# Kernel optimization log

Hardware: AMD Instinct MI355X
Metric: run time of the kernel (lower is better)

## Reference

```python
import jax, jax.numpy as jnp
import numpy as np

D_MODEL, FFN, N_EXP = 1024, 4096, 8
BS, L = 4, 2048


def setup_inputs() -> dict:
    key = jax.random.key(0)
    ks = jax.random.split(key, 7)
    s = 0.02
    return {
        "x": jax.random.normal(ks[0], (BS, L, D_MODEL), dtype=jnp.float32),
        "gate_w": s * jax.random.normal(ks[1], (D_MODEL, N_EXP), dtype=jnp.float32),
        "gate_b": jnp.zeros((N_EXP,), dtype=jnp.float32),
        "W1": s * jax.random.normal(ks[2], (N_EXP, D_MODEL, FFN), dtype=jnp.float32),
        "b1": jnp.zeros((N_EXP, FFN), dtype=jnp.float32),
        "W2": s * jax.random.normal(ks[3], (N_EXP, FFN, D_MODEL), dtype=jnp.float32),
        "b2": jnp.zeros((N_EXP, D_MODEL), dtype=jnp.float32),
    }


def reference(x, gate_w, gate_b, W1, b1, W2, b2):
    # gate logits [bs, l, E]; NOTE: original applies Softmax(dim=1) -> over seq dim
    logits = jnp.einsum("bld,de->ble", x, gate_w) + gate_b
    probs = jax.nn.softmax(logits, axis=1)  # faithful to nn.Softmax(dim=1)
    idx = jnp.argmax(probs, axis=-1)  # top-1 expert per token, [bs, l]
    # topk_weights are computed in the original but never applied to output.
    out = jnp.zeros_like(x)
    for e in range(N_EXP):  # fixed small expert loop (structurally distinct weights)
        h = jax.nn.gelu(jnp.einsum("bld,df->blf", x, W1[e]) + b1[e], approximate=False)
        y = jnp.einsum("blf,fd->bld", h, W2[e]) + b2[e]
        out = out + jnp.where((idx == e)[..., None], y, jnp.float32(0.0))
    return out
```

## Files before the change

kernel.cpp:

```cpp
#include <hip/hip_runtime.h>
#include <hip/hip_bf16.h>

typedef unsigned short u16;
typedef unsigned int u32;

using bf16x8 = __attribute__((ext_vector_type(8))) short;
using f32x4  = __attribute__((ext_vector_type(4))) float;

static constexpr int TOK  = 8192;
static constexpr int SEQ  = 2048;
static constexpr int DM   = 1024;
static constexpr int FF   = 4096;
static constexpr int NE   = 8;
static constexpr int MAXT = 72;
static constexpr int KS2  = 4;
static constexpr int NWG1 = MAXT * (FF/128);
static constexpr int NWG2 = MAXT * (DM/128) * KS2;

static constexpr size_t O_LOGITS = 0;
static constexpr size_t O_M      = 262144;
static constexpr size_t O_Z      = O_M + 128;
static constexpr size_t O_CNT    = O_Z + 128;
static constexpr size_t O_CUR    = O_CNT + 64;
static constexpr size_t O_OFF    = O_CUR + 64;
static constexpr size_t O_DESC   = 263168;
static constexpr size_t O_PERM   = 266240;
static constexpr size_t O_IDX    = 299008;
static constexpr size_t O_XG     = 524288;
static constexpr size_t O_W1T    = O_XG  + (size_t)TOK*DM*2;
static constexpr size_t O_W2T    = O_W1T + (size_t)NE*DM*FF*2;
static constexpr size_t O_H      = O_W2T + (size_t)NE*DM*FF*2;

__device__ __forceinline__ u16 f2bf(float f){
  __hip_bfloat16 h = __float2bfloat16(f);
  return *reinterpret_cast<u16*>(&h);
}

__device__ __forceinline__ void gld_lds16(const void* g, void* l){
  __builtin_amdgcn_global_load_lds((const __attribute__((address_space(1))) void*)g,
                                   (__attribute__((address_space(3))) void*)l, 16, 0, 0);
}

__device__ __forceinline__ float gelu_f(float v){
  float u = v * fmaf(v*v, 0.044715f, 1.0f) * 0.7978845608f;
  float ex = __builtin_amdgcn_exp2f(u * -2.885390082f);
  return v * __builtin_amdgcn_rcpf(1.0f + ex);
}

__global__ void k_gate(const float* __restrict__ x, const float* __restrict__ gw,
                       const float* __restrict__ gb, float* __restrict__ logits){
  __shared__ float sgw[NE*DM];
  for (int i = threadIdx.x; i < DM*NE; i += 256){
    int d = i >> 3, e = i & 7;
    sgw[e*DM + d] = gw[i];
  }
  __syncthreads();
  int wave = threadIdx.x >> 6, lane = threadIdx.x & 63;
  int t = blockIdx.x * 4 + wave;
  const float4* xr = (const float4*)(x + (size_t)t * DM);
  float acc[NE];
#pragma unroll
  for (int e = 0; e < NE; ++e) acc[e] = 0.f;
#pragma unroll
  for (int k = 0; k < 4; ++k){
    int v4 = k*64 + lane;
    float4 v = xr[v4];
#pragma unroll
    for (int e = 0; e < NE; ++e){
      const float4 g = *(const float4*)&sgw[e*DM + v4*4];
      acc[e] = fmaf(v.x, g.x, fmaf(v.y, g.y, fmaf(v.z, g.z, fmaf(v.w, g.w, acc[e]))));
    }
  }
#pragma unroll
  for (int off = 32; off; off >>= 1)
#pragma unroll
    for (int e = 0; e < NE; ++e) acc[e] += __shfl_xor(acc[e], off);
  if (lane == 0){
#pragma unroll
    for (int e = 0; e < NE; ++e) logits[(size_t)t*NE + e] = acc[e] + gb[e];
  }
}

__global__ void k_lse(const float* __restrict__ logits, float* __restrict__ mOut,
                      float* __restrict__ zOut){
  int be = blockIdx.x;
  int b = be >> 3, e = be & 7;
  const float* base = logits + ((size_t)b*SEQ)*NE + e;
  float m = -INFINITY;
  for (int l = threadIdx.x; l < SEQ; l += 256) m = fmaxf(m, base[(size_t)l*NE]);
  __shared__ float red[8];
#pragma unroll
  for (int off = 32; off; off >>= 1) m = fmaxf(m, __shfl_xor(m, off));
  if ((threadIdx.x & 63) == 0) red[threadIdx.x >> 6] = m;
  __syncthreads();
  m = fmaxf(fmaxf(red[0], red[1]), fmaxf(red[2], red[3]));
  float s = 0.f;
  for (int l = threadIdx.x; l < SEQ; l += 256) s += expf(base[(size_t)l*NE] - m);
#pragma unroll
  for (int off = 32; off; off >>= 1) s += __shfl_xor(s, off);
  if ((threadIdx.x & 63) == 0) red[4 + (threadIdx.x >> 6)] = s;
  __syncthreads();
  if (threadIdx.x == 0){ mOut[be] = m; zOut[be] = red[4]+red[5]+red[6]+red[7]; }
}

__global__ void k_route(const float* __restrict__ logits, const float* __restrict__ m,
                        const float* __restrict__ z, u32* __restrict__ cnt,
                        int* __restrict__ idx){
  int t = blockIdx.x*256 + threadIdx.x;
  int b = t >> 11;
  const float* lr = logits + (size_t)t*NE;
  float best = -INFINITY; int be = 0;
#pragma unroll
  for (int e = 0; e < NE; ++e){
    float p = expf(lr[e] - m[b*NE + e]) / z[b*NE + e];
    if (p > best){ best = p; be = e; }
  }
  idx[t] = be;
  atomicAdd(&cnt[be], 1u);
}

__global__ void k_plan(const u32* __restrict__ cnt, int* __restrict__ off,
                       int4* __restrict__ desc, u32* __restrict__ cur){
  if (threadIdx.x == 0){
    int offs[NE+1]; int o = 0;
    for (int e = 0; e < NE; ++e){ offs[e] = o; o += (int)cnt[e]; }
    offs[NE] = o;
    int nt = 0;
    for (int e = 0; e < NE; ++e){
      int c = (int)cnt[e];
      for (int s = 0; s < c; s += 128)
        desc[nt++] = make_int4(e, offs[e] + s, min(128, c - s), 0);
      off[e] = offs[e]; cur[e] = 0u;
    }
    off[NE] = offs[NE];
    for (int i = nt; i < MAXT; ++i) desc[i] = make_int4(-1, 0, 0, 0);
  }
}

__global__ void k_scatter(const int* __restrict__ idx, const int* __restrict__ off,
                          u32* __restrict__ cur, int* __restrict__ perm){
  int t = blockIdx.x*256 + threadIdx.x;
  int e = idx[t];
  int pos = off[e] + (int)atomicAdd(&cur[e], 1u);
  perm[pos] = t;
}

__global__ void k_gather(const float* __restrict__ x, const int* __restrict__ perm,
                         const int* __restrict__ idx, const float* __restrict__ b2,
                         u16* __restrict__ Xg, float* __restrict__ out){
  int p = blockIdx.x;
  int t = perm[p];
  int e = idx[t];
  const float4* src = (const float4*)(x + (size_t)t*DM);
  float4 v = src[threadIdx.x];
  uint2 o;
  o.x = (u32)f2bf(v.x) | ((u32)f2bf(v.y) << 16);
  o.y = (u32)f2bf(v.z) | ((u32)f2bf(v.w) << 16);
  *(uint2*)(Xg + (size_t)p*DM + threadIdx.x*4) = o;
  float4 bv = ((const float4*)(b2 + (size_t)e*DM))[threadIdx.x];
  ((float4*)(out + (size_t)t*DM))[threadIdx.x] = bv;
}

__global__ void k_trans(const float* __restrict__ in, u16* __restrict__ out,
                        int R, int C){
  __shared__ float tile[64][65];
  int e = blockIdx.z;
  int r0 = blockIdx.x*64, c0 = blockIdx.y*64;
  const float* src = in + ((size_t)e*R + r0)*C + c0;
  int lr = threadIdx.x >> 4, lc = (threadIdx.x & 15) * 4;
#pragma unroll
  for (int i = 0; i < 4; ++i){
    float4 v = *(const float4*)(src + (size_t)(lr + i*16)*C + lc);
    tile[lr + i*16][lc+0] = v.x; tile[lr + i*16][lc+1] = v.y;
    tile[lr + i*16][lc+2] = v.z; tile[lr + i*16][lc+3] = v.w;
  }
  __syncthreads();
  u16* dst = out + ((size_t)e*C + c0)*R + r0;
  int rr = (threadIdx.x & 7) * 8;
  int ocb = threadIdx.x >> 3;
#pragma unroll
  for (int p = 0; p < 2; ++p){
    int oc = ocb + p*32;
    u16 w[8];
#pragma unroll
    for (int k = 0; k < 8; ++k) w[k] = f2bf(tile[rr + k][oc]);
    uint4 o;
    o.x = (u32)w[0] | ((u32)w[1] << 16);
    o.y = (u32)w[2] | ((u32)w[3] << 16);
    o.z = (u32)w[4] | ((u32)w[5] << 16);
    o.w = (u32)w[6] | ((u32)w[7] << 16);
    *(uint4*)(dst + (size_t)oc*R + rr) = o;
  }
}


__global__ __launch_bounds__(512) void k_ffn1(const u16* __restrict__ Xg,
    const u16* __restrict__ W1T, const float* __restrict__ b1,
    u16* __restrict__ H, const int4* __restrict__ desc){
  int pid = blockIdx.x;
  int pid_sw = (pid & 7) * (NWG1/8) + (pid >> 3);
  int ng  = pid_sw / (MAXT*8);
  int rem = pid_sw - ng*(MAXT*8);
  int mt  = rem >> 3;
  int n0  = (ng*8 + (rem & 7)) * 128;
  int4 dd = desc[mt];
  int e = dd.x; if (e < 0) return;
  int m0 = dd.y, valid = dd.z;
  __shared__ __align__(16) u16 lA[2][128*64];
  __shared__ __align__(16) u16 lB[2][128*64];
  int tid = threadIdx.x, lane = tid & 63, wave = tid >> 6;
  int wr = wave >> 1, wc = wave & 1;
  const u16* Bsrc = W1T + ((size_t)e*FF + n0)*DM;
  f32x4 acc[2][4] = {};

  auto stage = [&](int buf, int kt){
    int k0 = kt * 64;
#pragma unroll
    for (int c = 0; c < 2; ++c){
      int idx = tid + c*512;
      int r = idx >> 3, s = idx & 7;
      int sp = (s ^ (r & 7)) * 8;
      int ra = m0 + r; if (ra > TOK-1) ra = TOK-1;
      gld_lds16(Xg   + (size_t)ra*DM + k0 + sp, (char*)&lA[buf][0] + idx*16);
      gld_lds16(Bsrc + (size_t)r *DM + k0 + sp, (char*)&lB[buf][0] + idx*16);
    }
  };

  stage(0, 0);
  __syncthreads();
  const int KT = DM / 64;
  for (int kt = 0; kt < KT; ++kt){
    int cur = kt & 1;
    if (kt + 1 < KT) stage(cur ^ 1, kt + 1);
    const char* cA = (const char*)&lA[cur][0];
    const char* cB = (const char*)&lB[cur][0];
    bf16x8 a[2][2], b[4][2];
#pragma unroll
    for (int m = 0; m < 2; ++m){
      int R = wr*32 + m*16 + (lane & 15);
#pragma unroll
      for (int h = 0; h < 2; ++h){
        int slot = (h*4 + (lane >> 4)) ^ (R & 7);
        a[m][h] = *(const bf16x8*)(cA + R*128 + slot*16);
      }
    }
#pragma unroll
    for (int n = 0; n < 4; ++n){
      int R = wc*64 + n*16 + (lane & 15);
#pragma unroll
      for (int h = 0; h < 2; ++h){
        int slot = (h*4 + (lane >> 4)) ^ (R & 7);
        b[n][h] = *(const bf16x8*)(cB + R*128 + slot*16);
      }
    }
#pragma unroll
    for (int m = 0; m < 2; ++m)
#pragma unroll
      for (int n = 0; n < 4; ++n){
        acc[m][n] = __builtin_amdgcn_mfma_f32_16x16x32_bf16(a[m][0], b[n][0], acc[m][n], 0,0,0);
        acc[m][n] = __builtin_amdgcn_mfma_f32_16x16x32_bf16(a[m][1], b[n][1], acc[m][n], 0,0,0);
      }
    __syncthreads();
  }

#pragma unroll
  for (int n = 0; n < 4; ++n){
    int col = n0 + wc*64 + n*16 + (lane & 15);
    float bias = b1[(size_t)e*FF + col];
#pragma unroll
    for (int m = 0; m < 2; ++m){
      int rbase = wr*32 + m*16 + ((lane >> 4) << 2);
#pragma unroll
      for (int j = 0; j < 4; ++j){
        int rit = rbase + j;
        if (rit < valid){
          float v = acc[m][n][j] + bias;
          H[(size_t)(m0 + rit)*FF + col] = f2bf(gelu_f(v));
        }
      }
    }
  }
}

__global__ __launch_bounds__(512) void k_ffn2(const u16* __restrict__ H,
    const u16* __restrict__ W2T, float* __restrict__ out,
    const int4* __restrict__ desc, const int* __restrict__ perm){
  int pid = blockIdx.x;
  int pid_sw = (pid & 7) * (NWG2/8) + (pid >> 3);
  int ks  = pid_sw / (MAXT*8);
  int rem = pid_sw - ks*(MAXT*8);
  int mt  = rem >> 3;
  int n0  = (rem & 7) * 128;
  int4 dd = desc[mt];
  int e = dd.x; if (e < 0) return;
  int m0 = dd.y, valid = dd.z;
  __shared__ __align__(16) u16 lA[2][128*64];
  __shared__ __align__(16) u16 lB[2][128*64];
  int tid = threadIdx.x, lane = tid & 63, wave = tid >> 6;
  int wr = wave >> 1, wc = wave & 1;
  const u16* Bsrc = W2T + ((size_t)e*DM + n0)*FF;
  const int kbase = ks * (FF/KS2);
  f32x4 acc[2][4] = {};

  auto stage = [&](int buf, int kt){
    int k0 = kbase + kt * 64;
#pragma unroll
    for (int c = 0; c < 2; ++c){
      int idx = tid + c*512;
      int r = idx >> 3, s = idx & 7;
      int sp = (s ^ (r & 7)) * 8;
      int ra = m0 + r; if (ra > TOK-1) ra = TOK-1;
      gld_lds16(H    + (size_t)ra*FF + k0 + sp, (char*)&lA[buf][0] + idx*16);
      gld_lds16(Bsrc + (size_t)r *FF + k0 + sp, (char*)&lB[buf][0] + idx*16);
    }
  };

  stage(0, 0);
  __syncthreads();
  const int KT = (FF/KS2) / 64;
  for (int kt = 0; kt < KT; ++kt){
    int cur = kt & 1;
    if (kt + 1 < KT) stage(cur ^ 1, kt + 1);
    const char* cA = (const char*)&lA[cur][0];
    const char* cB = (const char*)&lB[cur][0];
    bf16x8 a[2][2], b[4][2];
#pragma unroll
    for (int m = 0; m < 2; ++m){
      int R = wr*32 + m*16 + (lane & 15);
#pragma unroll
      for (int h = 0; h < 2; ++h){
        int slot = (h*4 + (lane >> 4)) ^ (R & 7);
        a[m][h] = *(const bf16x8*)(cA + R*128 + slot*16);
      }
    }
#pragma unroll
    for (int n = 0; n < 4; ++n){
      int R = wc*64 + n*16 + (lane & 15);
#pragma unroll
      for (int h = 0; h < 2; ++h){
        int slot = (h*4 + (lane >> 4)) ^ (R & 7);
        b[n][h] = *(const bf16x8*)(cB + R*128 + slot*16);
      }
    }
#pragma unroll
    for (int m = 0; m < 2; ++m)
#pragma unroll
      for (int n = 0; n < 4; ++n){
        acc[m][n] = __builtin_amdgcn_mfma_f32_16x16x32_bf16(a[m][0], b[n][0], acc[m][n], 0,0,0);
        acc[m][n] = __builtin_amdgcn_mfma_f32_16x16x32_bf16(a[m][1], b[n][1], acc[m][n], 0,0,0);
      }
    __syncthreads();
  }

#pragma unroll
  for (int m = 0; m < 2; ++m){
#pragma unroll
    for (int j = 0; j < 4; ++j){
      int rit = wr*32 + m*16 + ((lane >> 4) << 2) + j;
      if (rit < valid){
        int tok = perm[m0 + rit];
#pragma unroll
        for (int n = 0; n < 4; ++n){
          int col = n0 + wc*64 + n*16 + (lane & 15);
          unsafeAtomicAdd(&out[(size_t)tok*DM + col], acc[m][n][j]);
        }
      }
    }
  }
}

extern "C" void kernel_launch(void* const* d_in, const int* in_sizes, int n_in,
                              void* d_out, int out_size, void* d_ws, size_t ws_size,
                              hipStream_t stream){
  const float* x   = (const float*)d_in[0];
  const float* gw  = (const float*)d_in[1];
  const float* gb  = (const float*)d_in[2];
  const float* W1  = (const float*)d_in[3];
  const float* b1  = (const float*)d_in[4];
  const float* W2  = (const float*)d_in[5];
  const float* b2  = (const float*)d_in[6];
  float* out = (float*)d_out;
  char* ws = (char*)d_ws;

  float* logits = (float*)(ws + O_LOGITS);
  float* mArr   = (float*)(ws + O_M);
  float* zArr   = (float*)(ws + O_Z);
  u32*   cnt    = (u32*)  (ws + O_CNT);
  u32*   cur    = (u32*)  (ws + O_CUR);
  int*   off    = (int*)  (ws + O_OFF);
  int4*  desc   = (int4*) (ws + O_DESC);
  int*   perm   = (int*)  (ws + O_PERM);
  int*   idx    = (int*)  (ws + O_IDX);
  u16*   Xg     = (u16*)  (ws + O_XG);
  u16*   W1T    = (u16*)  (ws + O_W1T);
  u16*   W2T    = (u16*)  (ws + O_W2T);
  u16*   Hbuf   = (u16*)  (ws + O_H);

  hipMemsetAsync(ws + O_CNT, 0, 128, stream);

  k_gate   <<<TOK/4, 256, 0, stream>>>(x, gw, gb, logits);
  k_lse    <<<32,    256, 0, stream>>>(logits, mArr, zArr);
  k_route  <<<TOK/256, 256, 0, stream>>>(logits, mArr, zArr, cnt, idx);
  k_plan   <<<1,     64,  0, stream>>>(cnt, off, desc, cur);
  k_scatter<<<TOK/256, 256, 0, stream>>>(idx, off, cur, perm);
  k_gather <<<TOK,   256, 0, stream>>>(x, perm, idx, b2, Xg, out);
  k_trans  <<<dim3(DM/64, FF/64, NE), 256, 0, stream>>>(W1, W1T, DM, FF);
  k_trans  <<<dim3(FF/64, DM/64, NE), 256, 0, stream>>>(W2, W2T, FF, DM);
  k_ffn1   <<<NWG1,  512, 0, stream>>>(Xg, W1T, b1, Hbuf, desc);
  k_ffn2   <<<NWG2,  512, 0, stream>>>(Hbuf, W2T, out, desc, perm);
}
```

Measured before the change: 490.5 us.

## Enlarge FFN GEMM tiles to 256x256 with interleaved LDS loads and MFMA scheduling

Both grouped expert GEMMs move from 128x128 to 256x256 output tiles: expert segments are split into 256-row chunks and each wave now computes a 128x64 sub-tile. The main loop is reordered so B and half of A are read from LDS before the next stage's global-to-LDS prefetch is issued. The second half of A is loaded between MFMA groups, with s_setprio around the MFMAs and explicit waitcnt/barriers. The aim is higher arithmetic intensity and fewer redundant weight reads, at the cost of 128KB LDS per block, large register use, and more wasted rows in partially filled expert tiles.

```diff
diff --git a/kernel.cpp b/kernel.cpp
--- a/kernel.cpp
+++ b/kernel.cpp
@@ -12,10 +12,10 @@
 static constexpr int DM   = 1024;
 static constexpr int FF   = 4096;
 static constexpr int NE   = 8;
-static constexpr int MAXT = 72;
+static constexpr int MAXT2= 40;
 static constexpr int KS2  = 4;
-static constexpr int NWG1 = MAXT * (FF/128);
-static constexpr int NWG2 = MAXT * (DM/128) * KS2;
+static constexpr int NWG1 = MAXT2 * (FF/256);
+static constexpr int NWG2 = MAXT2 * (DM/256) * KS2;
 
 static constexpr size_t O_LOGITS = 0;
 static constexpr size_t O_M      = 262144;
@@ -23,7 +23,7 @@
 static constexpr size_t O_CNT    = O_Z + 128;
 static constexpr size_t O_CUR    = O_CNT + 64;
 static constexpr size_t O_OFF    = O_CUR + 64;
-static constexpr size_t O_DESC   = 263168;
+static constexpr size_t O_DESC2  = 264320;
 static constexpr size_t O_PERM   = 266240;
 static constexpr size_t O_IDX    = 299008;
 static constexpr size_t O_XG     = 524288;
@@ -120,20 +120,20 @@
 }
 
 __global__ void k_plan(const u32* __restrict__ cnt, int* __restrict__ off,
-                       int4* __restrict__ desc, u32* __restrict__ cur){
+                       int4* __restrict__ desc2, u32* __restrict__ cur){
   if (threadIdx.x == 0){
     int offs[NE+1]; int o = 0;
     for (int e = 0; e < NE; ++e){ offs[e] = o; o += (int)cnt[e]; }
     offs[NE] = o;
-    int nt = 0;
+    int nt2 = 0;
     for (int e = 0; e < NE; ++e){
       int c = (int)cnt[e];
-      for (int s = 0; s < c; s += 128)
-        desc[nt++] = make_int4(e, offs[e] + s, min(128, c - s), 0);
+      for (int s = 0; s < c; s += 256)
+        desc2[nt2++] = make_int4(e, offs[e] + s, min(256, c - s), 0);
       off[e] = offs[e]; cur[e] = 0u;
     }
     off[NE] = offs[NE];
-    for (int i = nt; i < MAXT; ++i) desc[i] = make_int4(-1, 0, 0, 0);
+    for (int i = nt2; i < MAXT2; ++i) desc2[i] = make_int4(-1, 0, 0, 0);
   }
 }
 
@@ -194,29 +194,31 @@
 }
 
 
-__global__ __launch_bounds__(512) void k_ffn1(const u16* __restrict__ Xg,
+__global__ __launch_bounds__(512, 2) void k_ffn1(const u16* __restrict__ Xg,
     const u16* __restrict__ W1T, const float* __restrict__ b1,
-    u16* __restrict__ H, const int4* __restrict__ desc){
+    u16* __restrict__ H, const int4* __restrict__ desc2){
   int pid = blockIdx.x;
   int pid_sw = (pid & 7) * (NWG1/8) + (pid >> 3);
-  int ng  = pid_sw / (MAXT*8);
-  int rem = pid_sw - ng*(MAXT*8);
-  int mt  = rem >> 3;
-  int n0  = (ng*8 + (rem & 7)) * 128;
-  int4 dd = desc[mt];
+  int mt = pid_sw % MAXT2;
+  int n0 = (pid_sw / MAXT2) * 256;
+  int4 dd = desc2[mt];
   int e = dd.x; if (e < 0) return;
   int m0 = dd.y, valid = dd.z;
-  __shared__ __align__(16) u16 lA[2][128*64];
-  __shared__ __align__(16) u16 lB[2][128*64];
+
+  __shared__ __align__(16) u16 lA[2][256*64];
+  __shared__ __align__(16) u16 lB[2][256*64];
+
   int tid = threadIdx.x, lane = tid & 63, wave = tid >> 6;
-  int wr = wave >> 1, wc = wave & 1;
+  int wm = wave >> 2, wn = wave & 3;
   const u16* Bsrc = W1T + ((size_t)e*FF + n0)*DM;
-  f32x4 acc[2][4] = {};
-
-  auto stage = [&](int buf, int kt){
+
+  f32x4 acc[8][4] = {};
+  bf16x8 a[4][2], b[4][2];
+
+  auto STAGE = [&](int buf, int kt){
     int k0 = kt * 64;
 #pragma unroll
-    for (int c = 0; c < 2; ++c){
+    for (int c = 0; c < 4; ++c){
       int idx = tid + c*512;
       int r = idx >> 3, s = idx & 7;
       int sp = (s ^ (r & 7)) * 8;
@@ -225,56 +227,77 @@
       gld_lds16(Bsrc + (size_t)r *DM + k0 + sp, (char*)&lB[buf][0] + idx*16);
     }
   };
-
-  stage(0, 0);
-  __syncthreads();
+  auto LDA = [&](const char* cA, int mh){
+#pragma unroll
+    for (int f = 0; f < 4; ++f){
+      int R = wm*128 + mh*64 + f*16 + (lane & 15);
+#pragma unroll
+      for (int h = 0; h < 2; ++h){
+        int slot = (h*4 + (lane >> 4)) ^ (R & 7);
+        a[f][h] = *(const bf16x8*)(cA + R*128 + slot*16);
+      }
+    }
+  };
+  auto LDB = [&](const char* cB){
+#pragma unroll
+    for (int g = 0; g < 4; ++g){
+      int R = wn*64 + g*16 + (lane & 15);
+#pragma unroll
+      for (int h = 0; h < 2; ++h){
+        int slot = (h*4 + (lane >> 4)) ^ (R & 7);
+        b[g][h] = *(const bf16x8*)(cB + R*128 + slot*16);
+      }
+    }
+  };
+  auto MM = [&](int mh, int nh){
+    __builtin_amdgcn_s_setprio(1);
+#pragma unroll
+    for (int f = 0; f < 4; ++f)
+#pragma unroll
+      for (int g = 0; g < 2; ++g){
+        int G = nh*2 + g;
+        acc[mh*4+f][G] = __builtin_amdgcn_mfma_f32_16x16x32_bf16(a[f][0], b[G][0], acc[mh*4+f][G], 0,0,0);
+        acc[mh*4+f][G] = __builtin_amdgcn_mfma_f32_16x16x32_bf16(a[f][1], b[G][1], acc[mh*4+f][G], 0,0,0);
+      }
+    __builtin_amdgcn_s_setprio(0);
+  };
+
+  STAGE(0, 0);
+  __builtin_amdgcn_sched_barrier(0);
+  asm volatile("s_waitcnt vmcnt(0)");
+  __builtin_amdgcn_sched_barrier(0);
+  __builtin_amdgcn_s_barrier();
+
   const int KT = DM / 64;
   for (int kt = 0; kt < KT; ++kt){
     int cur = kt & 1;
-    if (kt + 1 < KT) stage(cur ^ 1, kt + 1);
     const char* cA = (const char*)&lA[cur][0];
     const char* cB = (const char*)&lB[cur][0];
-    bf16x8 a[2][2], b[4][2];
-#pragma unroll
-    for (int m = 0; m < 2; ++m){
-      int R = wr*32 + m*16 + (lane & 15);
-#pragma unroll
-      for (int h = 0; h < 2; ++h){
-        int slot = (h*4 + (lane >> 4)) ^ (R & 7);
-        a[m][h] = *(const bf16x8*)(cA + R*128 + slot*16);
-      }
-    }
-#pragma unroll
-    for (int n = 0; n < 4; ++n){
-      int R = wc*64 + n*16 + (lane & 15);
-#pragma unroll
-      for (int h = 0; h < 2; ++h){
-        int slot = (h*4 + (lane >> 4)) ^ (R & 7);
-        b[n][h] = *(const bf16x8*)(cB + R*128 + slot*16);
-      }
-    }
-#pragma unroll
-    for (int m = 0; m < 2; ++m)
-#pragma unroll
-      for (int n = 0; n < 4; ++n){
-        acc[m][n] = __builtin_amdgcn_mfma_f32_16x16x32_bf16(a[m][0], b[n][0], acc[m][n], 0,0,0);
-        acc[m][n] = __builtin_amdgcn_mfma_f32_16x16x32_bf16(a[m][1], b[n][1], acc[m][n], 0,0,0);
-      }
-    __syncthreads();
-  }
-
-#pragma unroll
-  for (int n = 0; n < 4; ++n){
-    int col = n0 + wc*64 + n*16 + (lane & 15);
+    LDB(cB);
+    LDA(cA, 0);
+    if (kt + 1 < KT) STAGE(cur ^ 1, kt + 1);
+    __builtin_amdgcn_s_barrier();
+    MM(0, 0); MM(0, 1);
+    LDA(cA, 1);
+    MM(1, 1); MM(1, 0);
+    __builtin_amdgcn_sched_barrier(0);
+    asm volatile("s_waitcnt vmcnt(0)");
+    __builtin_amdgcn_sched_barrier(0);
+    __builtin_amdgcn_s_barrier();
+  }
+
+#pragma unroll
+  for (int fn = 0; fn < 4; ++fn){
+    int col = n0 + wn*64 + fn*16 + (lane & 15);
     float bias = b1[(size_t)e*FF + col];
 #pragma unroll
-    for (int m = 0; m < 2; ++m){
-      int rbase = wr*32 + m*16 + ((lane >> 4) << 2);
+    for (int fm = 0; fm < 8; ++fm){
+      int rbase = wm*128 + fm*16 + ((lane >> 4) << 2);
 #pragma unroll
       for (int j = 0; j < 4; ++j){
         int rit = rbase + j;
         if (rit < valid){
-          float v = acc[m][n][j] + bias;
+          float v = acc[fm][fn][j] + bias;
           H[(size_t)(m0 + rit)*FF + col] = f2bf(gelu_f(v));
         }
       }
@@ -282,30 +305,34 @@
   }
 }
 
-__global__ __launch_bounds__(512) void k_ffn2(const u16* __restrict__ H,
+__global__ __launch_bounds__(512, 2) void k_ffn2(const u16* __restrict__ H,
     const u16* __restrict__ W2T, float* __restrict__ out,
-    const int4* __restrict__ desc, const int* __restrict__ perm){
+    const int4* __restrict__ desc2, const int* __restrict__ perm){
   int pid = blockIdx.x;
   int pid_sw = (pid & 7) * (NWG2/8) + (pid >> 3);
-  int ks  = pid_sw / (MAXT*8);
-  int rem = pid_sw - ks*(MAXT*8);
-  int mt  = rem >> 3;
-  int n0  = (rem & 7) * 128;
-  int4 dd = desc[mt];
+  int mt = pid_sw % MAXT2;
+  int rest = pid_sw / MAXT2;
+  int ks = rest >> 2;
+  int n0 = (rest & 3) * 256;
+  int4 dd = desc2[mt];
   int e = dd.x; if (e < 0) return;
   int m0 = dd.y, valid = dd.z;
-  __shared__ __align__(16) u16 lA[2][128*64];
-  __shared__ __align__(16) u16 lB[2][128*64];
+
+  __shared__ __align__(16) u16 lA[2][256*64];
+  __shared__ __align__(16) u16 lB[2][256*64];
+
   int tid = threadIdx.x, lane = tid & 63, wave = tid >> 6;
-  int wr = wave >> 1, wc = wave & 1;
+  int wm = wave >> 2, wn = wave & 3;
   const u16* Bsrc = W2T + ((size_t)e*DM + n0)*FF;
   const int kbase = ks * (FF/KS2);
-  f32x4 acc[2][4] = {};
-
-  auto stage = [&](int buf, int kt){
+
+  f32x4 acc[8][4] = {};
+  bf16x8 a[4][2], b[4][2];
+
+  auto STAGE = [&](int buf, int kt){
     int k0 = kbase + kt * 64;
 #pragma unroll
-    for (int c = 0; c < 2; ++c){
+    for (int c = 0; c < 4; ++c){
       int idx = tid + c*512;
       int r = idx >> 3, s = idx & 7;
       int sp = (s ^ (r & 7)) * 8;
@@ -314,55 +341,76 @@
       gld_lds16(Bsrc + (size_t)r *FF + k0 + sp, (char*)&lB[buf][0] + idx*16);
     }
   };
-
-  stage(0, 0);
-  __syncthreads();
+  auto LDA = [&](const char* cA, int mh){
+#pragma unroll
+    for (int f = 0; f < 4; ++f){
+      int R = wm*128 + mh*64 + f*16 + (lane & 15);
+#pragma unroll
+      for (int h = 0; h < 2; ++h){
+        int slot = (h*4 + (lane >> 4)) ^ (R & 7);
+        a[f][h] = *(const bf16x8*)(cA + R*128 + slot*16);
+      }
+    }
+  };
+  auto LDB = [&](const char* cB){
+#pragma unroll
+    for (int g = 0; g < 4; ++g){
+      int R = wn*64 + g*16 + (lane & 15);
+#pragma unroll
+      for (int h = 0; h < 2; ++h){
+        int slot = (h*4 + (lane >> 4)) ^ (R & 7);
+        b[g][h] = *(const bf16x8*)(cB + R*128 + slot*16);
+      }
+    }
+  };
+  auto MM = [&](int mh, int nh){
+    __builtin_amdgcn_s_setprio(1);
+#pragma unroll
+    for (int f = 0; f < 4; ++f)
+#pragma unroll
+      for (int g = 0; g < 2; ++g){
+        int G = nh*2 + g;
+        acc[mh*4+f][G] = __builtin_amdgcn_mfma_f32_16x16x32_bf16(a[f][0], b[G][0], acc[mh*4+f][G], 0,0,0);
+        acc[mh*4+f][G] = __builtin_amdgcn_mfma_f32_16x16x32_bf16(a[f][1], b[G][1], acc[mh*4+f][G], 0,0,0);
+      }
+    __builtin_amdgcn_s_setprio(0);
+  };
+
+  STAGE(0, 0);
+  __builtin_amdgcn_sched_barrier(0);
+  asm volatile("s_waitcnt vmcnt(0)");
+  __builtin_amdgcn_sched_barrier(0);
+  __builtin_amdgcn_s_barrier();
+
   const int KT = (FF/KS2) / 64;
   for (int kt = 0; kt < KT; ++kt){
     int cur = kt & 1;
-    if (kt + 1 < KT) stage(cur ^ 1, kt + 1);
     const char* cA = (const char*)&lA[cur][0];
     const char* cB = (const char*)&lB[cur][0];
-    bf16x8 a[2][2], b[4][2];
-#pragma unroll
-    for (int m = 0; m < 2; ++m){
-      int R = wr*32 + m*16 + (lane & 15);
-#pragma unroll
-      for (int h = 0; h < 2; ++h){
-        int slot = (h*4 + (lane >> 4)) ^ (R & 7);
-        a[m][h] = *(const bf16x8*)(cA + R*128 + slot*16);
-      }
-    }
-#pragma unroll
-    for (int n = 0; n < 4; ++n){
-      int R = wc*64 + n*16 + (lane & 15);
-#pragma unroll
-      for (int h = 0; h < 2; ++h){
-        int slot = (h*4 + (lane >> 4)) ^ (R & 7);
-        b[n][h] = *(const bf16x8*)(cB + R*128 + slot*16);
-      }
-    }
-#pragma unroll
-    for (int m = 0; m < 2; ++m)
-#pragma unroll
-      for (int n = 0; n < 4; ++n){
-        acc[m][n] = __builtin_amdgcn_mfma_f32_16x16x32_bf16(a[m][0], b[n][0], acc[m][n], 0,0,0);
-        acc[m][n] = __builtin_amdgcn_mfma_f32_16x16x32_bf16(a[m][1], b[n][1], acc[m][n], 0,0,0);
-      }
-    __syncthreads();
-  }
-
-#pragma unroll
-  for (int m = 0; m < 2; ++m){
+    LDB(cB);
+    LDA(cA, 0);
+    if (kt + 1 < KT) STAGE(cur ^ 1, kt + 1);
+    __builtin_amdgcn_s_barrier();
+    MM(0, 0); MM(0, 1);
+    LDA(cA, 1);
+    MM(1, 1); MM(1, 0);
+    __builtin_amdgcn_sched_barrier(0);
+    asm volatile("s_waitcnt vmcnt(0)");
+    __builtin_amdgcn_sched_barrier(0);
+    __builtin_amdgcn_s_barrier();
+  }
+
+#pragma unroll
+  for (int fm = 0; fm < 8; ++fm){
 #pragma unroll
     for (int j = 0; j < 4; ++j){
-      int rit = wr*32 + m*16 + ((lane >> 4) << 2) + j;
+      int rit = wm*128 + fm*16 + ((lane >> 4) << 2) + j;
       if (rit < valid){
         int tok = perm[m0 + rit];
 #pragma unroll
-        for (int n = 0; n < 4; ++n){
-          int col = n0 + wc*64 + n*16 + (lane & 15);
-          unsafeAtomicAdd(&out[(size_t)tok*DM + col], acc[m][n][j]);
+        for (int fn = 0; fn < 4; ++fn){
+          int col = n0 + wn*64 + fn*16 + (lane & 15);
+          unsafeAtomicAdd(&out[(size_t)tok*DM + col], acc[fm][fn][j]);
         }
       }
     }
@@ -388,7 +436,7 @@
   u32*   cnt    = (u32*)  (ws + O_CNT);
   u32*   cur    = (u32*)  (ws + O_CUR);
   int*   off    = (int*)  (ws + O_OFF);
-  int4*  desc   = (int4*) (ws + O_DESC);
+  int4*  desc2  = (int4*) (ws + O_DESC2);
   int*   perm   = (int*)  (ws + O_PERM);
   int*   idx    = (int*)  (ws + O_IDX);
   u16*   Xg     = (u16*)  (ws + O_XG);
@@ -401,11 +449,11 @@
   k_gate   <<<TOK/4, 256, 0, stream>>>(x, gw, gb, logits);
   k_lse    <<<32,    256, 0, stream>>>(logits, mArr, zArr);
   k_route  <<<TOK/256, 256, 0, stream>>>(logits, mArr, zArr, cnt, idx);
-  k_plan   <<<1,     64,  0, stream>>>(cnt, off, desc, cur);
+  k_plan   <<<1,     64,  0, stream>>>(cnt, off, desc2, cur);
   k_scatter<<<TOK/256, 256, 0, stream>>>(idx, off, cur, perm);
   k_gather <<<TOK,   256, 0, stream>>>(x, perm, idx, b2, Xg, out);
   k_trans  <<<dim3(DM/64, FF/64, NE), 256, 0, stream>>>(W1, W1T, DM, FF);
   k_trans  <<<dim3(FF/64, DM/64, NE), 256, 0, stream>>>(W2, W2T, FF, DM);
-  k_ffn1   <<<NWG1,  512, 0, stream>>>(Xg, W1T, b1, Hbuf, desc);
-  k_ffn2   <<<NWG2,  512, 0, stream>>>(Hbuf, W2T, out, desc, perm);
-}
+  k_ffn1   <<<NWG1,  512, 0, stream>>>(Xg, W1T, b1, Hbuf, desc2);
+  k_ffn2   <<<NWG2,  512, 0, stream>>>(Hbuf, W2T, out, desc2, perm);
+}
```

New measurement: 543.2 us. 1.11x slower.
